# Optimization experiments

Measured on AMD Instinct MI355X. Metric: run time of the kernel, lower is better.

The kernel has to match this reference:

```python
import jax, jax.numpy as jnp
import numpy as np

PARTS_NUM = 16
MAX_INIT = -100.0  # torch scatter_reduce amax include_self initial value


def setup_inputs() -> dict:
    key = jax.random.key(0)
    k1, k2 = jax.random.split(key)
    x = jax.random.normal(k1, (32, 256, 30, 16, 16), dtype=jnp.float32)
    part_labels = jax.random.randint(k2, (32, 30, 16, 16), 0, PARTS_NUM, dtype=jnp.int64)
    return {"x": x, "part_labels": part_labels}


def reference(x, part_labels):
    n, c, s, h, w = x.shape
    ns = n * s
    hw = h * w
    P = PARTS_NUM
    # feat: (ns*hw, c) -- channels-last for efficient segment reductions
    feat = jnp.transpose(x, (0, 2, 3, 4, 1)).reshape(ns * hw, c)
    labels = part_labels.reshape(ns, hw).astype(jnp.int32)
    # one flat segment id per (frame, part) pair
    seg = (labels + jnp.arange(ns, dtype=jnp.int32)[:, None] * P).reshape(ns * hw)
    num_seg = ns * P
    pooled_sum = jax.ops.segment_sum(feat, seg, num_segments=num_seg)          # (ns*P, c)
    pooled_count = jax.ops.segment_sum(jnp.ones((ns * hw,), feat.dtype), seg,
                                       num_segments=num_seg)                   # (ns*P,)
    pooled_max = jax.ops.segment_max(feat, seg, num_segments=num_seg)          # (ns*P, c)
    valid = (pooled_count > 0)[:, None]                                        # (ns*P, 1)
    pooled_mean = pooled_sum / jnp.maximum(pooled_count, 1.0)[:, None]
    # torch scatter_reduce includes initial -100.0 in the amax; empty parts -> 0
    pooled_max = jnp.where(valid, jnp.maximum(pooled_max, MAX_INIT), 0.0)
    pooled = pooled_mean + pooled_max                                          # (ns*P, c)
    # -> (n, c, s, P)
    return jnp.transpose(pooled.reshape(n, s, P, c), (0, 3, 1, 2))
```

## Files before the change

### kernel.cpp

```cpp
#include <hip/hip_runtime.h>


#define C_DIM 256
#define S_DIM 30
#define P_NUM 16
#define HW 256
#define CH_PER_BLK 32
#define TS 260

__global__ __launch_bounds__(256, 4)
void partpp_pool_kernel(const float* __restrict__ x,
                        const int* __restrict__ labels,
                        float* __restrict__ out) {
    __shared__ float tile[CH_PER_BLK * TS];
    __shared__ int rank[HW];
    __shared__ int counts[P_NUM], cursor[P_NUM], offs[P_NUM + 1];

    const int t   = threadIdx.x;
    const int b   = blockIdx.x;
    const int f   = b >> 3;
    const int q   = b & 7;
    const int ch0 = q * CH_PER_BLK;
    const int n   = f / S_DIM;
    const int s   = f - n * S_DIM;

    const int lab = labels[f * HW + t];

    const size_t xbase = ((size_t)(n * C_DIM + ch0) * S_DIM + s) * HW;
    const int col = t & 63;
    float4 v[8];
    #pragma unroll
    for (int j = 0; j < 8; ++j) {
        const int row = j * 4 + (t >> 6);
        v[j] = *(const float4*)(x + xbase + (size_t)row * (S_DIM * HW) + col * 4);
    }

    if (t < P_NUM) { counts[t] = 0; cursor[t] = 0; }
    __syncthreads();
    atomicAdd(&counts[lab], 1);
    __syncthreads();
    if (t == 0) {
        int acc = 0;
        #pragma unroll
        for (int p = 0; p < P_NUM; ++p) { offs[p] = acc; acc += counts[p]; }
        offs[P_NUM] = acc;
    }
    __syncthreads();
    rank[t] = offs[lab] + atomicAdd(&cursor[lab], 1);
    __syncthreads();

    const int4 rk = *(const int4*)&rank[col * 4];
    #pragma unroll
    for (int j = 0; j < 8; ++j) {
        const int row = j * 4 + (t >> 6);
        float* rp = &tile[row * TS];
        rp[rk.x] = v[j].x;
        rp[rk.y] = v[j].y;
        rp[rk.z] = v[j].z;
        rp[rk.w] = v[j].w;
    }
    __syncthreads();

    const int ch  = t >> 3;
    const int sub = t & 7;
    const float* rowp = &tile[ch * TS];

    float res[2];
    #pragma unroll
    for (int pi = 0; pi < 2; ++pi) {
        const int p  = sub * 2 + pi;
        const int jb = offs[p];
        const int je = offs[p + 1];
        float sum = 0.0f;
        float mx  = -3.0e38f;
        for (int j = jb; j < je; ++j) {
            const float vv = rowp[j];
            sum += vv;
            mx = fmaxf(mx, vv);
        }
        res[pi] = (je > jb) ? (sum / (float)(je - jb) + fmaxf(mx, -100.0f)) : 0.0f;
    }

    float* op = out + ((size_t)(n * C_DIM + ch0 + ch) * S_DIM + s) * P_NUM + sub * 2;
    *(float2*)op = make_float2(res[0], res[1]);
}

extern "C" void kernel_launch(void* const* d_in, const int* in_sizes, int n_in,
                              void* d_out, int out_size, void* d_ws, size_t ws_size,
                              hipStream_t stream) {
    const float* x      = (const float*)d_in[0];
    const int*   labels = (const int*)d_in[1];
    float*       out    = (float*)d_out;

    dim3 grid(960 * 8), block(256);
    hipLaunchKernelGGL(partpp_pool_kernel, grid, block, 0, stream, x, labels, out);
}
```

Before: 336.4 us.

## Halve channels per block, pad segments to float4, one thread per part

```diff
diff --git a/kernel.cpp b/kernel.cpp
--- a/kernel.cpp
+++ b/kernel.cpp
@@ -5,22 +5,22 @@
 #define S_DIM 30
 #define P_NUM 16
 #define HW 256
-#define CH_PER_BLK 32
-#define TS 260
+#define CH_PER_BLK 16
+#define TS 304
 
-__global__ __launch_bounds__(256, 4)
+__global__ __launch_bounds__(256, 8)
 void partpp_pool_kernel(const float* __restrict__ x,
                         const int* __restrict__ labels,
                         float* __restrict__ out) {
     __shared__ float tile[CH_PER_BLK * TS];
-    __shared__ int rank[HW];
+    __shared__ unsigned short rank[HW];
     __shared__ int counts[P_NUM], cursor[P_NUM], offs[P_NUM + 1];
 
     const int t   = threadIdx.x;
     const int b   = blockIdx.x;
-    const int f   = b >> 3;
-    const int q   = b & 7;
-    const int ch0 = q * CH_PER_BLK;
+    const int f   = b >> 4;
+    const int g   = b & 15;
+    const int ch0 = g * CH_PER_BLK;
     const int n   = f / S_DIM;
     const int s   = f - n * S_DIM;
 
@@ -28,9 +28,9 @@
 
     const size_t xbase = ((size_t)(n * C_DIM + ch0) * S_DIM + s) * HW;
     const int col = t & 63;
-    float4 v[8];
+    float4 v[4];
     #pragma unroll
-    for (int j = 0; j < 8; ++j) {
+    for (int j = 0; j < 4; ++j) {
         const int row = j * 4 + (t >> 6);
         v[j] = *(const float4*)(x + xbase + (size_t)row * (S_DIM * HW) + col * 4);
     }
@@ -42,16 +42,19 @@
     if (t == 0) {
         int acc = 0;
         #pragma unroll
-        for (int p = 0; p < P_NUM; ++p) { offs[p] = acc; acc += counts[p]; }
+        for (int p = 0; p < P_NUM; ++p) {
+            offs[p] = acc;
+            acc += (counts[p] + 3) & ~3;
+        }
         offs[P_NUM] = acc;
     }
     __syncthreads();
-    rank[t] = offs[lab] + atomicAdd(&cursor[lab], 1);
+    rank[t] = (unsigned short)(offs[lab] + atomicAdd(&cursor[lab], 1));
     __syncthreads();
 
-    const int4 rk = *(const int4*)&rank[col * 4];
+    const ushort4 rk = *(const ushort4*)&rank[col * 4];
     #pragma unroll
-    for (int j = 0; j < 8; ++j) {
+    for (int j = 0; j < 4; ++j) {
         const int row = j * 4 + (t >> 6);
         float* rp = &tile[row * TS];
         rp[rk.x] = v[j].x;
@@ -61,28 +64,29 @@
     }
     __syncthreads();
 
-    const int ch  = t >> 3;
-    const int sub = t & 7;
-    const float* rowp = &tile[ch * TS];
+    const int ch = t >> 4;
+    const int p  = t & 15;
+    float* rowp = &tile[ch * TS];
+    const int jb   = offs[p];
+    const int cnt  = counts[p];
+    const int len4 = (cnt + 3) & ~3;
 
-    float res[2];
-    #pragma unroll
-    for (int pi = 0; pi < 2; ++pi) {
-        const int p  = sub * 2 + pi;
-        const int jb = offs[p];
-        const int je = offs[p + 1];
-        float sum = 0.0f;
-        float mx  = -3.0e38f;
-        for (int j = jb; j < je; ++j) {
-            const float vv = rowp[j];
-            sum += vv;
-            mx = fmaxf(mx, vv);
-        }
-        res[pi] = (je > jb) ? (sum / (float)(je - jb) + fmaxf(mx, -100.0f)) : 0.0f;
+    for (int k = jb + cnt; k < jb + len4; ++k) rowp[k] = -100.0f;
+
+    float sum = 0.0f;
+    float mx  = -3.0e38f;
+    const float4* rp4 = (const float4*)(rowp + jb);
+    const int n4 = len4 >> 2;
+    for (int q = 0; q < n4; ++q) {
+        const float4 vv = rp4[q];
+        sum += vv.x + vv.y + vv.z + vv.w;
+        mx = fmaxf(fmaxf(mx, fmaxf(vv.x, vv.y)), fmaxf(vv.z, vv.w));
     }
+    sum += 100.0f * (float)(len4 - cnt);
 
-    float* op = out + ((size_t)(n * C_DIM + ch0 + ch) * S_DIM + s) * P_NUM + sub * 2;
-    *(float2*)op = make_float2(res[0], res[1]);
+    const float res = (cnt > 0) ? (sum / (float)cnt + fmaxf(mx, -100.0f)) : 0.0f;
+
+    out[((size_t)(n * C_DIM + ch0 + ch) * S_DIM + s) * P_NUM + p] = res;
 }
 
 extern "C" void kernel_launch(void* const* d_in, const int* in_sizes, int n_in,
@@ -92,6 +96,6 @@
     const int*   labels = (const int*)d_in[1];
     float*       out    = (float*)d_out;
 
-    dim3 grid(960 * 8), block(256);
+    dim3 grid(960 * 16), block(256);
     hipLaunchKernelGGL(partpp_pool_kernel, grid, block, 0, stream, x, labels, out);
 }
```

Result: no change. 333.8 us (-0.8%).
